# Kernel tuning notes

Measured on AMD Instinct MI355X. Metric: run time of the kernel, lower is better.

Reference implementation:

```python
import jax, jax.numpy as jnp
import numpy as np

N = 50000
E = 600000
IN_C = 128
HID = 128
OUT_C = 2


def setup_inputs() -> dict:
    key = jax.random.key(0)
    ks = jax.random.split(key, 16)
    x = jax.random.normal(ks[0], (N, IN_C), dtype=jnp.float32)
    edge_index = jax.random.randint(ks[1], (2, E), 0, N, dtype=jnp.int64)
    s = 0.05
    # policy_net: Linear(2*in, 64) -> ReLU -> Linear(64, 1) -> Sigmoid
    W_p1 = jax.random.normal(ks[2], (64, 2 * IN_C), dtype=jnp.float32) * s
    b_p1 = jnp.zeros((64,), dtype=jnp.float32)
    W_p2 = jax.random.normal(ks[3], (1, 64), dtype=jnp.float32) * s
    b_p2 = jnp.zeros((1,), dtype=jnp.float32)
    # GCNConv weights (lin without bias + separate bias, PyG convention)
    W1 = jax.random.normal(ks[4], (HID, IN_C), dtype=jnp.float32) * s
    b1 = jnp.zeros((HID,), dtype=jnp.float32)
    W2 = jax.random.normal(ks[5], (HID, HID), dtype=jnp.float32) * s
    b2 = jnp.zeros((HID,), dtype=jnp.float32)
    W_lin = jax.random.normal(ks[6], (OUT_C, HID), dtype=jnp.float32) * s
    b_lin = jnp.zeros((OUT_C,), dtype=jnp.float32)
    return {"x": x, "edge_index": edge_index, "W_p1": W_p1, "b_p1": b_p1,
            "W_p2": W_p2, "b_p2": b_p2, "W1": W1, "b1": b1, "W2": W2,
            "b2": b2, "W_lin": W_lin, "b_lin": b_lin}


def gcn_conv(x, src, dst, edge_weight, W, b, n_nodes):
    # PyG GCNConv with normalize=True, add_self_loops=True, given edge_weight.
    loop = jnp.arange(n_nodes, dtype=src.dtype)
    s = jnp.concatenate([src, loop])
    d = jnp.concatenate([dst, loop])
    w = jnp.concatenate([edge_weight, jnp.ones((n_nodes,), x.dtype)])
    deg = jax.ops.segment_sum(w, d, num_segments=n_nodes)
    dinv = jnp.where(deg > 0, jax.lax.rsqrt(jnp.where(deg > 0, deg, 1.0)), 0.0)
    norm = dinv[s] * w * dinv[d]  # [E+N]
    xl = x @ W.T  # [N, out]
    msg = norm[:, None] * xl[s]  # gather + scale
    agg = jax.ops.segment_sum(msg, d, num_segments=n_nodes)
    return agg + b


def reference(x, edge_index, W_p1, b_p1, W_p2, b_p2, W1, b1, W2, b2, W_lin, b_lin):
    src, dst = edge_index[0], edge_index[1]
    # edge-weight policy MLP on gathered, concatenated endpoint features
    cat_feat = jnp.concatenate([x[src], x[dst]], axis=1)  # [E, 2*in]
    h = jax.nn.relu(cat_feat @ W_p1.T + b_p1)
    edge_weight = jax.nn.sigmoid(h @ W_p2.T + b_p2)[:, 0]  # [E]
    x1 = jax.nn.relu(gcn_conv(x, src, dst, edge_weight, W1, b1, N))
    x2 = jax.nn.relu(gcn_conv(x1, src, dst, edge_weight, W2, b2, N))
    out = x2 @ W_lin.T + b_lin
    return jax.nn.sigmoid(out)
```

## Files before the change

### kernel.cpp

```cpp
#include <hip/hip_runtime.h>
#include <hip/hip_bf16.h>

#define NN 50000
#define NE 600000
#define CPAD 16

typedef __attribute__((ext_vector_type(8))) short short8;
typedef __attribute__((ext_vector_type(8))) _Float16 half8;
typedef __attribute__((ext_vector_type(4))) float floatx4;

__device__ __forceinline__ short bf16_bits(float v) {
    __hip_bfloat16 h = __float2bfloat16(v);
    return *reinterpret_cast<short*>(&h);
}

__device__ __forceinline__ void stage_w(const short* __restrict__ src, short* lds) {
    int t = threadIdx.x;
#pragma unroll
    for (int i = 0; i < 8; ++i) {
        int gci = t + i * 256;
        int row = gci >> 4, ci = gci & 15;
        short8 v = *(const short8*)(src + gci * 8);
        *(short8*)(lds + row * 128 + ((ci ^ (row & 7)) << 3)) = v;
    }
}

__global__ void k_init_cvt(const int* __restrict__ raw, int* __restrict__ count,
                           int* __restrict__ flag, int* __restrict__ bsums,
                           const float* __restrict__ wp1,
                           const float* __restrict__ w1, const float* __restrict__ w2,
                           __hip_bfloat16* __restrict__ wcatb, __hip_bfloat16* __restrict__ w1b,
                           __hip_bfloat16* __restrict__ w2b) {
    int i = blockIdx.x * blockDim.x + threadIdx.x;
    if (i < NN) {
        count[(size_t)i * CPAD] = 0;
    }
    if (i < 128) bsums[i] = 0;
    if (i < 16384) {
        int r = i >> 7, c = i & 127;
        float v = (r < 64) ? wp1[r * 256 + c] : wp1[(r - 64) * 256 + 128 + c];
        wcatb[i] = __float2bfloat16(v);
    } else if (i < 32768) {
        w1b[i - 16384] = __float2bfloat16(w1[i - 16384]);
    } else if (i < 49152) {
        w2b[i - 32768] = __float2bfloat16(w2[i - 32768]);
    }
    if (blockIdx.x == 0) {
        if (threadIdx.x == 0) *flag = 0;
        __syncthreads();
        int any = 0;
        for (int j = threadIdx.x; j < 1024; j += 256) any |= raw[2 * j + 1];
        if (any) atomicOr(flag, 1);
    }
}

#define GCNT 293
#define GG 782
__global__ __launch_bounds__(256) void k_uv_cnt(
    const float* __restrict__ x, const __hip_bfloat16* __restrict__ Wb,
    const float* __restrict__ bp1, _Float16* __restrict__ uvh,
    __hip_bfloat16* __restrict__ xb, const int* __restrict__ raw,
    const int* __restrict__ flag, int* __restrict__ count, int* __restrict__ rank) {
    if (blockIdx.x < GCNT) {
        const bool f32 = (*flag) != 0;
        const long long* r64 = (const long long*)raw;
        int gid = blockIdx.x * 256 + threadIdx.x;
        int e0 = gid * 8;
        if (e0 + 8 <= NE) {
            int dd[8];
            if (f32) {
#pragma unroll
                for (int k = 0; k < 8; ++k) dd[k] = raw[NE + e0 + k];
            } else {
#pragma unroll
                for (int k = 0; k < 8; ++k) dd[k] = (int)r64[NE + e0 + k];
            }
            int rk[8];
#pragma unroll
            for (int k = 0; k < 8; ++k) rk[k] = atomicAdd(&count[(size_t)dd[k] * CPAD], 1);
#pragma unroll
            for (int k = 0; k < 8; ++k) rank[e0 + k] = rk[k];
        } else {
            for (int e = e0; e < NE; ++e) {
                int d = f32 ? raw[NE + e] : (int)r64[NE + e];
                rank[e] = atomicAdd(&count[(size_t)d * CPAD], 1);
            }
        }
        return;
    }
    __shared__ short wlds[16384];
    stage_w((const short*)Wb, wlds);
    __syncthreads();

    const int lane = threadIdx.x & 63;
    const int wave = threadIdx.x >> 6;
    const int col = lane & 15;
    const int quad = lane >> 4;

    int tile = (blockIdx.x - GCNT) * 4 + wave;
    if (tile >= NN / 16) return;
    int base = tile * 16;

    short8 bfrag[4][8];
    const int rx = col & 7;
#pragma unroll
    for (int tt = 0; tt < 8; ++tt) {
        int row = tt * 16 + col;
#pragma unroll
        for (int kk = 0; kk < 4; ++kk)
            bfrag[kk][tt] = *(const short8*)(wlds + row * 128 + (((kk * 4 + quad) ^ rx) << 3));
    }

    floatx4 acc[8];
#pragma unroll
    for (int t = 0; t < 8; ++t) acc[t] = (floatx4){0.f, 0.f, 0.f, 0.f};
#pragma unroll
    for (int kk = 0; kk < 4; ++kk) {
        const float* xrow = x + (size_t)(base + col) * 128 + kk * 32 + quad * 8;
        float4 f0 = ((const float4*)xrow)[0];
        float4 f1 = ((const float4*)xrow)[1];
        short8 afrag;
        afrag[0] = bf16_bits(f0.x); afrag[1] = bf16_bits(f0.y);
        afrag[2] = bf16_bits(f0.z); afrag[3] = bf16_bits(f0.w);
        afrag[4] = bf16_bits(f1.x); afrag[5] = bf16_bits(f1.y);
        afrag[6] = bf16_bits(f1.z); afrag[7] = bf16_bits(f1.w);
        *(short8*)((short*)xb + (size_t)(base + col) * 128 + kk * 32 + quad * 8) = afrag;
#pragma unroll
        for (int tt = 0; tt < 8; ++tt)
            acc[tt] = __builtin_amdgcn_mfma_f32_16x16x32_bf16(afrag, bfrag[kk][tt], acc[tt], 0, 0, 0);
    }
#pragma unroll
    for (int tt = 0; tt < 8; ++tt) {
        int n = tt * 16 + col;
        float badd = (tt >= 4) ? bp1[n - 64] : 0.f;
#pragma unroll
        for (int r = 0; r < 4; ++r) {
            int row = base + quad * 4 + r;
            uvh[(size_t)row * 128 + n] = (_Float16)(acc[tt][r] + badd);
        }
    }
}

__global__ __launch_bounds__(512) void k_scan_rowptr(
    const int* __restrict__ count, int* __restrict__ bsums, int* __restrict__ rowptr) {
    __shared__ int s[512];
    __shared__ int red[512];
    int tid = threadIdx.x, bid = blockIdx.x;
    int i = bid * 512 + tid;
    s[tid] = (i < NN) ? count[(size_t)i * CPAD] : 0;
    __syncthreads();
    for (int off = 1; off < 512; off <<= 1) {
        int t = (tid >= off) ? s[tid - off] : 0;
        __syncthreads();
        s[tid] += t;
        __syncthreads();
    }
    if (tid == 511) atomicExch(&bsums[bid], s[511] + 1);
    int part = 0;
    for (int j = tid; j < bid; j += 512) {
        int v;
        do { v = atomicAdd(&bsums[j], 0); } while (v == 0);
        part += v - 1;
    }
    red[tid] = part;
    __syncthreads();
    for (int off = 256; off > 0; off >>= 1) {
        if (tid < off) red[tid] += red[tid + off];
        __syncthreads();
    }
    int prefix = red[0];
    if (i < NN) rowptr[i + 1] = s[tid] + prefix;
    if (bid == 0 && tid == 0) rowptr[0] = 0;
}

#define GPOL 9375
__global__ __launch_bounds__(256) void k_pol_fill(
    const int* __restrict__ raw, const int* __restrict__ flag,
    const int* __restrict__ rank, const int* __restrict__ rowptr,
    const _Float16* __restrict__ uvh, const float* __restrict__ wp2,
    const float* __restrict__ bp2, int2* __restrict__ meta) {
    const bool f32 = (*flag) != 0;
    const long long* r64 = (const long long*)raw;
    int pb = blockIdx.x;
    int wave = threadIdx.x >> 6, lane = threadIdx.x & 63;
    int g = lane >> 3, c = lane & 7;
    int e1 = pb * 64 + wave * 16 + g;
    int e2 = e1 + 8;
    int s1, d1, s2, d2;
    if (f32) {
        s1 = raw[e1]; d1 = raw[NE + e1];
        s2 = raw[e2]; d2 = raw[NE + e2];
    } else {
        s1 = (int)r64[e1]; d1 = (int)r64[NE + e1];
        s2 = (int)r64[e2]; d2 = (int)r64[NE + e2];
    }
    half8 u1 = *(const half8*)(uvh + (size_t)s1 * 128 + c * 8);
    half8 v1 = *(const half8*)(uvh + (size_t)d1 * 128 + 64 + c * 8);
    half8 u2 = *(const half8*)(uvh + (size_t)s2 * 128 + c * 8);
    half8 v2 = *(const half8*)(uvh + (size_t)d2 * 128 + 64 + c * 8);
    float w2v[8];
    const float4* w2p = (const float4*)(wp2 + c * 8);
    float4 wa = w2p[0], wb = w2p[1];
    w2v[0] = wa.x; w2v[1] = wa.y; w2v[2] = wa.z; w2v[3] = wa.w;
    w2v[4] = wb.x; w2v[5] = wb.y; w2v[6] = wb.z; w2v[7] = wb.w;
    float b2 = bp2[0];
    float p1 = 0.f, p2 = 0.f;
#pragma unroll
    for (int j = 0; j < 8; ++j) {
        float h1 = (float)u1[j] + (float)v1[j];
        float h2 = (float)u2[j] + (float)v2[j];
        h1 = h1 > 0.f ? h1 : 0.f;
        h2 = h2 > 0.f ? h2 : 0.f;
        p1 += h1 * w2v[j];
        p2 += h2 * w2v[j];
    }
    p1 += __shfl_xor(p1, 1, 64); p2 += __shfl_xor(p2, 1, 64);
    p1 += __shfl_xor(p1, 2, 64); p2 += __shfl_xor(p2, 2, 64);
    p1 += __shfl_xor(p1, 4, 64); p2 += __shfl_xor(p2, 4, 64);
    if (c == 0) {
        float ew1 = 1.f / (1.f + __expf(-(p1 + b2)));
        float ew2 = 1.f / (1.f + __expf(-(p2 + b2)));
        int rk1 = rank[e1], rk2 = rank[e2];
        int rb1 = rowptr[d1], rb2 = rowptr[d2];
        meta[rb1 + rk1] = make_int2(s1, __float_as_int(ew1));
        meta[rb2 + rk2] = make_int2(s2, __float_as_int(ew2));
    }
}

template <bool CDEG>
__global__ __launch_bounds__(256) void k_gemm(
    const __hip_bfloat16* __restrict__ A, const __hip_bfloat16* __restrict__ Wb,
    const int* __restrict__ rowptr, const int2* __restrict__ meta,
    float* __restrict__ deg, _Float16* __restrict__ xlh) {
    __shared__ short wlds[16384];
    stage_w((const short*)Wb, wlds);
    __syncthreads();

    const int lane = threadIdx.x & 63;
    const int wave = threadIdx.x >> 6;
    const int col = lane & 15;
    const int quad = lane >> 4;

    int tile = blockIdx.x * 4 + wave;
    if (tile >= NN / 16) return;
    int base = tile * 16;

    short8 bfrag[4][8];
    const int rx = col & 7;
#pragma unroll
    for (int tt = 0; tt < 8; ++tt) {
        int row = tt * 16 + col;
#pragma unroll
        for (int kk = 0; kk < 4; ++kk)
            bfrag[kk][tt] = *(const short8*)(wlds + row * 128 + (((kk * 4 + quad) ^ rx) << 3));
    }
    const short* xs = (const short*)A;

    floatx4 acc[8];
#pragma unroll
    for (int t = 0; t < 8; ++t) acc[t] = (floatx4){0.f, 0.f, 0.f, 0.f};
#pragma unroll
    for (int kk = 0; kk < 4; ++kk) {
        short8 afrag = *(const short8*)(xs + (size_t)(base + col) * 128 + kk * 32 + quad * 8);
#pragma unroll
        for (int tt = 0; tt < 8; ++tt)
            acc[tt] = __builtin_amdgcn_mfma_f32_16x16x32_bf16(afrag, bfrag[kk][tt], acc[tt], 0, 0, 0);
    }
    float di[4];
    if (CDEG) {
        int rn = base + col;
        int beg = rowptr[rn], end = rowptr[rn + 1];
        float sdeg = 0.f;
        for (int p = beg + quad; p < end; p += 4) sdeg += __int_as_float(meta[p].y);
        sdeg += __shfl_xor(sdeg, 16, 64);
        sdeg += __shfl_xor(sdeg, 32, 64);
        float dv = 1.f + sdeg;
        if (quad == 0) deg[rn] = dv;
#pragma unroll
        for (int r = 0; r < 4; ++r) di[r] = rsqrtf(__shfl(dv, quad * 4 + r, 64));
    } else {
#pragma unroll
        for (int r = 0; r < 4; ++r) di[r] = rsqrtf(deg[base + quad * 4 + r]);
    }
#pragma unroll
    for (int tt = 0; tt < 8; ++tt) {
        int n = tt * 16 + col;
#pragma unroll
        for (int r = 0; r < 4; ++r) {
            int row = base + quad * 4 + r;
            xlh[(size_t)row * 128 + n] = (_Float16)(di[r] * acc[tt][r]);
        }
    }
}

__device__ __forceinline__ void scatter_core(
    const int* __restrict__ rowptr, const int2* __restrict__ meta,
    const _Float16* __restrict__ xlh, int wid, int g, int c, float acc[8]) {
    int beg = rowptr[wid], end = rowptr[wid + 1];
    for (int p = beg + g; p < end; p += 16) {
        int2 m1 = meta[p];
        int2 m2 = (p + 4  < end) ? meta[p + 4]  : make_int2(m1.x, 0);
        int2 m3 = (p + 8  < end) ? meta[p + 8]  : make_int2(m1.x, 0);
        int2 m4 = (p + 12 < end) ? meta[p + 12] : make_int2(m1.x, 0);
        half8 r1 = *(const half8*)(xlh + (size_t)m1.x * 128 + c * 8);
        half8 r2 = *(const half8*)(xlh + (size_t)m2.x * 128 + c * 8);
        half8 r3 = *(const half8*)(xlh + (size_t)m3.x * 128 + c * 8);
        half8 r4 = *(const half8*)(xlh + (size_t)m4.x * 128 + c * 8);
        float c1 = __int_as_float(m1.y), c2 = __int_as_float(m2.y);
        float c3 = __int_as_float(m3.y), c4 = __int_as_float(m4.y);
#pragma unroll
        for (int j = 0; j < 8; ++j)
            acc[j] += c1 * (float)r1[j] + c2 * (float)r2[j] + c3 * (float)r3[j] + c4 * (float)r4[j];
    }
#pragma unroll
    for (int j = 0; j < 8; ++j) {
        acc[j] += __shfl_xor(acc[j], 16, 64);
        acc[j] += __shfl_xor(acc[j], 32, 64);
    }
}

__global__ __launch_bounds__(256) void k_scatter_mid(
    const int* __restrict__ rowptr, const int2* __restrict__ meta,
    const float* __restrict__ deg, const _Float16* __restrict__ xlh,
    const float* __restrict__ bias, __hip_bfloat16* __restrict__ xb2) {
    int wid = (blockIdx.x * blockDim.x + threadIdx.x) >> 6;
    int lane = threadIdx.x & 63;
    if (wid >= NN) return;
    int g = lane >> 4, c = lane & 15;
    float acc[8] = {0.f, 0.f, 0.f, 0.f, 0.f, 0.f, 0.f, 0.f};
    scatter_core(rowptr, meta, xlh, wid, g, c, acc);
    if (g == 0) {
        float dn = rsqrtf(deg[wid]);
        half8 sv = *(const half8*)(xlh + (size_t)wid * 128 + c * 8);
        const float4* bp = (const float4*)(bias + c * 8);
        float4 ba = bp[0], bb = bp[1];
        float bv[8] = {ba.x, ba.y, ba.z, ba.w, bb.x, bb.y, bb.z, bb.w};
        short8 o;
#pragma unroll
        for (int j = 0; j < 8; ++j) {
            float t = bv[j] + dn * ((float)sv[j] + acc[j]);
            t = t > 0.f ? t : 0.f;
            o[j] = bf16_bits(t);
        }
        *(short8*)((short*)xb2 + (size_t)wid * 128 + c * 8) = o;
    }
}

__global__ __launch_bounds__(256) void k_scatter_out(
    const int* __restrict__ rowptr, const int2* __restrict__ meta,
    const float* __restrict__ deg, const _Float16* __restrict__ xlh,
    const float* __restrict__ bias, const float* __restrict__ wlin,
    const float* __restrict__ blin, float* __restrict__ out) {
    int wid = (blockIdx.x * blockDim.x + threadIdx.x) >> 6;
    int lane = threadIdx.x & 63;
    if (wid >= NN) return;
    int g = lane >> 4, c = lane & 15;
    float acc[8] = {0.f, 0.f, 0.f, 0.f, 0.f, 0.f, 0.f, 0.f};
    scatter_core(rowptr, meta, xlh, wid, g, c, acc);
    if (g == 0) {
        float dn = rsqrtf(deg[wid]);
        half8 sv = *(const half8*)(xlh + (size_t)wid * 128 + c * 8);
        const float4* bp = (const float4*)(bias + c * 8);
        float4 ba = bp[0], bb = bp[1];
        float bv[8] = {ba.x, ba.y, ba.z, ba.w, bb.x, bb.y, bb.z, bb.w};
        float p0 = 0.f, p1 = 0.f;
#pragma unroll
        for (int j = 0; j < 8; ++j) {
            float t = bv[j] + dn * ((float)sv[j] + acc[j]);
            t = t > 0.f ? t : 0.f;
            p0 += t * wlin[c * 8 + j];
            p1 += t * wlin[128 + c * 8 + j];
        }
#pragma unroll
        for (int off = 1; off < 16; off <<= 1) {
            p0 += __shfl_xor(p0, off, 64);
            p1 += __shfl_xor(p1, off, 64);
        }
        if (c == 0) {
            out[wid * 2 + 0] = 1.f / (1.f + __expf(-(p0 + blin[0])));
            out[wid * 2 + 1] = 1.f / (1.f + __expf(-(p1 + blin[1])));
        }
    }
}


extern "C" void kernel_launch(void* const* d_in, const int* in_sizes, int n_in,
                              void* d_out, int out_size, void* d_ws, size_t ws_size,
                              hipStream_t stream) {
    const float* x = (const float*)d_in[0];
    const int* eidx_raw = (const int*)d_in[1];
    const float* W_p1 = (const float*)d_in[2];
    const float* b_p1 = (const float*)d_in[3];
    const float* W_p2 = (const float*)d_in[4];
    const float* b_p2 = (const float*)d_in[5];
    const float* W1 = (const float*)d_in[6];
    const float* b1 = (const float*)d_in[7];
    const float* W2 = (const float*)d_in[8];
    const float* b2 = (const float*)d_in[9];
    const float* W_lin = (const float*)d_in[10];
    const float* b_lin = (const float*)d_in[11];
    float* out = (float*)d_out;

    char* ws = (char*)d_ws;
    size_t off = 0;
    auto alloc = [&](size_t bytes) -> void* {
        off = (off + 255) & ~(size_t)255;
        void* p = ws + off;
        off += bytes;
        return p;
    };
    float* deg = (float*)alloc(NN * 4);
    int* rowptr = (int*)alloc((NN + 1) * 4);
    int* count = (int*)alloc((size_t)NN * CPAD * 4);
    int* flag = (int*)alloc(4);
    int* bsums = (int*)alloc(128 * 4);
    int* rank = (int*)alloc((size_t)NE * 4);
    int2* meta = (int2*)alloc((size_t)NE * 8);
    __hip_bfloat16* xb = (__hip_bfloat16*)alloc((size_t)NN * 128 * 2);
    _Float16* xlh = (_Float16*)alloc((size_t)NN * 128 * 2);
    _Float16* uvh = (_Float16*)alloc((size_t)NN * 128 * 2);
    __hip_bfloat16* wcatb = (__hip_bfloat16*)alloc(128 * 128 * 2);
    __hip_bfloat16* w1b = (__hip_bfloat16*)alloc(128 * 128 * 2);
    __hip_bfloat16* w2b = (__hip_bfloat16*)alloc(128 * 128 * 2);

    const int TB = 256;
    int gN = (NN + TB - 1) / TB;
    int gS = (NN + 3) / 4;

    k_init_cvt<<<gN, TB, 0, stream>>>(eidx_raw, count, flag, bsums, W_p1, W1, W2, wcatb, w1b, w2b);
    k_uv_cnt<<<GCNT + GG, TB, 0, stream>>>(x, wcatb, b_p1, uvh, xb, eidx_raw, flag, count, rank);
    k_scan_rowptr<<<98, 512, 0, stream>>>(count, bsums, rowptr);
    k_pol_fill<<<GPOL, TB, 0, stream>>>(eidx_raw, flag, rank, rowptr, uvh, W_p2, b_p2, meta);
    k_gemm<true><<<GG, TB, 0, stream>>>(xb, w1b, rowptr, meta, deg, xlh);
    k_scatter_mid<<<gS, TB, 0, stream>>>(rowptr, meta, deg, xlh, b1, xb);
    k_gemm<false><<<GG, TB, 0, stream>>>(xb, w2b, rowptr, meta, deg, xlh);
    k_scatter_out<<<gS, TB, 0, stream>>>(rowptr, meta, deg, xlh, b2, W_lin, b_lin, out);
}
```

Before: 235.5 us.

## Fuse first GCN GEMM into policy GEMM kernel and compute degrees via atomics

```diff
diff --git a/kernel.cpp b/kernel.cpp
--- a/kernel.cpp
+++ b/kernel.cpp
@@ -26,14 +26,15 @@
 }
 
 __global__ void k_init_cvt(const int* __restrict__ raw, int* __restrict__ count,
-                           int* __restrict__ flag, int* __restrict__ bsums,
-                           const float* __restrict__ wp1,
+                           float* __restrict__ degp, int* __restrict__ flag,
+                           int* __restrict__ bsums, const float* __restrict__ wp1,
                            const float* __restrict__ w1, const float* __restrict__ w2,
                            __hip_bfloat16* __restrict__ wcatb, __hip_bfloat16* __restrict__ w1b,
                            __hip_bfloat16* __restrict__ w2b) {
     int i = blockIdx.x * blockDim.x + threadIdx.x;
     if (i < NN) {
         count[(size_t)i * CPAD] = 0;
+        degp[(size_t)i * CPAD] = 1.0f;
     }
     if (i < 128) bsums[i] = 0;
     if (i < 16384) {
@@ -54,32 +55,33 @@
     }
 }
 
-#define GCNT 293
+#define GCNT 147
 #define GG 782
 __global__ __launch_bounds__(256) void k_uv_cnt(
-    const float* __restrict__ x, const __hip_bfloat16* __restrict__ Wb,
-    const float* __restrict__ bp1, _Float16* __restrict__ uvh,
-    __hip_bfloat16* __restrict__ xb, const int* __restrict__ raw,
-    const int* __restrict__ flag, int* __restrict__ count, int* __restrict__ rank) {
+    const float* __restrict__ x, const __hip_bfloat16* __restrict__ Wcat,
+    const __hip_bfloat16* __restrict__ W1b, const float* __restrict__ bp1,
+    _Float16* __restrict__ uvh, _Float16* __restrict__ xlh,
+    const int* __restrict__ raw, const int* __restrict__ flag,
+    int* __restrict__ count, int* __restrict__ rank) {
     if (blockIdx.x < GCNT) {
         const bool f32 = (*flag) != 0;
         const long long* r64 = (const long long*)raw;
         int gid = blockIdx.x * 256 + threadIdx.x;
-        int e0 = gid * 8;
-        if (e0 + 8 <= NE) {
-            int dd[8];
+        int e0 = gid * 16;
+        if (e0 + 16 <= NE) {
+            int dd[16];
             if (f32) {
 #pragma unroll
-                for (int k = 0; k < 8; ++k) dd[k] = raw[NE + e0 + k];
+                for (int k = 0; k < 16; ++k) dd[k] = raw[NE + e0 + k];
             } else {
 #pragma unroll
-                for (int k = 0; k < 8; ++k) dd[k] = (int)r64[NE + e0 + k];
-            }
-            int rk[8];
-#pragma unroll
-            for (int k = 0; k < 8; ++k) rk[k] = atomicAdd(&count[(size_t)dd[k] * CPAD], 1);
-#pragma unroll
-            for (int k = 0; k < 8; ++k) rank[e0 + k] = rk[k];
+                for (int k = 0; k < 16; ++k) dd[k] = (int)r64[NE + e0 + k];
+            }
+            int rk[16];
+#pragma unroll
+            for (int k = 0; k < 16; ++k) rk[k] = atomicAdd(&count[(size_t)dd[k] * CPAD], 1);
+#pragma unroll
+            for (int k = 0; k < 16; ++k) rank[e0 + k] = rk[k];
         } else {
             for (int e = e0; e < NE; ++e) {
                 int d = f32 ? raw[NE + e] : (int)r64[NE + e];
@@ -89,54 +91,79 @@
         return;
     }
     __shared__ short wlds[16384];
-    stage_w((const short*)Wb, wlds);
+    stage_w((const short*)Wcat, wlds);
     __syncthreads();
 
     const int lane = threadIdx.x & 63;
     const int wave = threadIdx.x >> 6;
     const int col = lane & 15;
     const int quad = lane >> 4;
+    const int rx = col & 7;
 
     int tile = (blockIdx.x - GCNT) * 4 + wave;
-    if (tile >= NN / 16) return;
+    if (tile >= NN / 16) tile = NN / 16 - 1;
     int base = tile * 16;
 
-    short8 bfrag[4][8];
-    const int rx = col & 7;
-#pragma unroll
-    for (int tt = 0; tt < 8; ++tt) {
-        int row = tt * 16 + col;
-#pragma unroll
-        for (int kk = 0; kk < 4; ++kk)
-            bfrag[kk][tt] = *(const short8*)(wlds + row * 128 + (((kk * 4 + quad) ^ rx) << 3));
-    }
-
-    floatx4 acc[8];
-#pragma unroll
-    for (int t = 0; t < 8; ++t) acc[t] = (floatx4){0.f, 0.f, 0.f, 0.f};
+    short8 af[4];
 #pragma unroll
     for (int kk = 0; kk < 4; ++kk) {
         const float* xrow = x + (size_t)(base + col) * 128 + kk * 32 + quad * 8;
         float4 f0 = ((const float4*)xrow)[0];
         float4 f1 = ((const float4*)xrow)[1];
-        short8 afrag;
-        afrag[0] = bf16_bits(f0.x); afrag[1] = bf16_bits(f0.y);
-        afrag[2] = bf16_bits(f0.z); afrag[3] = bf16_bits(f0.w);
-        afrag[4] = bf16_bits(f1.x); afrag[5] = bf16_bits(f1.y);
-        afrag[6] = bf16_bits(f1.z); afrag[7] = bf16_bits(f1.w);
-        *(short8*)((short*)xb + (size_t)(base + col) * 128 + kk * 32 + quad * 8) = afrag;
-#pragma unroll
-        for (int tt = 0; tt < 8; ++tt)
-            acc[tt] = __builtin_amdgcn_mfma_f32_16x16x32_bf16(afrag, bfrag[kk][tt], acc[tt], 0, 0, 0);
-    }
-#pragma unroll
-    for (int tt = 0; tt < 8; ++tt) {
-        int n = tt * 16 + col;
-        float badd = (tt >= 4) ? bp1[n - 64] : 0.f;
-#pragma unroll
-        for (int r = 0; r < 4; ++r) {
-            int row = base + quad * 4 + r;
-            uvh[(size_t)row * 128 + n] = (_Float16)(acc[tt][r] + badd);
+        short8 a;
+        a[0] = bf16_bits(f0.x); a[1] = bf16_bits(f0.y);
+        a[2] = bf16_bits(f0.z); a[3] = bf16_bits(f0.w);
+        a[4] = bf16_bits(f1.x); a[5] = bf16_bits(f1.y);
+        a[6] = bf16_bits(f1.z); a[7] = bf16_bits(f1.w);
+        af[kk] = a;
+    }
+
+    {
+        floatx4 acc[8];
+#pragma unroll
+        for (int t = 0; t < 8; ++t) acc[t] = (floatx4){0.f, 0.f, 0.f, 0.f};
+#pragma unroll
+        for (int kk = 0; kk < 4; ++kk) {
+#pragma unroll
+            for (int tt = 0; tt < 8; ++tt) {
+                short8 b = *(const short8*)(wlds + (tt * 16 + col) * 128 + (((kk * 4 + quad) ^ rx) << 3));
+                acc[tt] = __builtin_amdgcn_mfma_f32_16x16x32_bf16(af[kk], b, acc[tt], 0, 0, 0);
+            }
+        }
+#pragma unroll
+        for (int tt = 0; tt < 8; ++tt) {
+            int n = tt * 16 + col;
+            float badd = (tt >= 4) ? bp1[n - 64] : 0.f;
+#pragma unroll
+            for (int r = 0; r < 4; ++r) {
+                int row = base + quad * 4 + r;
+                uvh[(size_t)row * 128 + n] = (_Float16)(acc[tt][r] + badd);
+            }
+        }
+    }
+    __syncthreads();
+    stage_w((const short*)W1b, wlds);
+    __syncthreads();
+    {
+        floatx4 acc[8];
+#pragma unroll
+        for (int t = 0; t < 8; ++t) acc[t] = (floatx4){0.f, 0.f, 0.f, 0.f};
+#pragma unroll
+        for (int kk = 0; kk < 4; ++kk) {
+#pragma unroll
+            for (int tt = 0; tt < 8; ++tt) {
+                short8 b = *(const short8*)(wlds + (tt * 16 + col) * 128 + (((kk * 4 + quad) ^ rx) << 3));
+                acc[tt] = __builtin_amdgcn_mfma_f32_16x16x32_bf16(af[kk], b, acc[tt], 0, 0, 0);
+            }
+        }
+#pragma unroll
+        for (int tt = 0; tt < 8; ++tt) {
+            int n = tt * 16 + col;
+#pragma unroll
+            for (int r = 0; r < 4; ++r) {
+                int row = base + quad * 4 + r;
+                xlh[(size_t)row * 128 + n] = (_Float16)(acc[tt][r]);
+            }
         }
     }
 }
@@ -178,7 +205,7 @@
     const int* __restrict__ raw, const int* __restrict__ flag,
     const int* __restrict__ rank, const int* __restrict__ rowptr,
     const _Float16* __restrict__ uvh, const float* __restrict__ wp2,
-    const float* __restrict__ bp2, int2* __restrict__ meta) {
+    const float* __restrict__ bp2, int2* __restrict__ meta, float* __restrict__ degp) {
     const bool f32 = (*flag) != 0;
     const long long* r64 = (const long long*)raw;
     int pb = blockIdx.x;
@@ -224,14 +251,14 @@
         int rb1 = rowptr[d1], rb2 = rowptr[d2];
         meta[rb1 + rk1] = make_int2(s1, __float_as_int(ew1));
         meta[rb2 + rk2] = make_int2(s2, __float_as_int(ew2));
-    }
-}
-
-template <bool CDEG>
-__global__ __launch_bounds__(256) void k_gemm(
+        atomicAdd(&degp[(size_t)d1 * CPAD], ew1);
+        atomicAdd(&degp[(size_t)d2 * CPAD], ew2);
+    }
+}
+
+__global__ __launch_bounds__(256) void k_gemm2(
     const __hip_bfloat16* __restrict__ A, const __hip_bfloat16* __restrict__ Wb,
-    const int* __restrict__ rowptr, const int2* __restrict__ meta,
-    float* __restrict__ deg, _Float16* __restrict__ xlh) {
+    const float* __restrict__ degp, _Float16* __restrict__ xlh) {
     __shared__ short wlds[16384];
     stage_w((const short*)Wb, wlds);
     __syncthreads();
@@ -267,21 +294,8 @@
             acc[tt] = __builtin_amdgcn_mfma_f32_16x16x32_bf16(afrag, bfrag[kk][tt], acc[tt], 0, 0, 0);
     }
     float di[4];
-    if (CDEG) {
-        int rn = base + col;
-        int beg = rowptr[rn], end = rowptr[rn + 1];
-        float sdeg = 0.f;
-        for (int p = beg + quad; p < end; p += 4) sdeg += __int_as_float(meta[p].y);
-        sdeg += __shfl_xor(sdeg, 16, 64);
-        sdeg += __shfl_xor(sdeg, 32, 64);
-        float dv = 1.f + sdeg;
-        if (quad == 0) deg[rn] = dv;
-#pragma unroll
-        for (int r = 0; r < 4; ++r) di[r] = rsqrtf(__shfl(dv, quad * 4 + r, 64));
-    } else {
-#pragma unroll
-        for (int r = 0; r < 4; ++r) di[r] = rsqrtf(deg[base + quad * 4 + r]);
-    }
+#pragma unroll
+    for (int r = 0; r < 4; ++r) di[r] = rsqrtf(degp[(size_t)(base + quad * 4 + r) * CPAD]);
 #pragma unroll
     for (int tt = 0; tt < 8; ++tt) {
         int n = tt * 16 + col;
@@ -290,6 +304,37 @@
             int row = base + quad * 4 + r;
             xlh[(size_t)row * 128 + n] = (_Float16)(di[r] * acc[tt][r]);
         }
+    }
+}
+
+__device__ __forceinline__ void scatter_core_u(
+    const int* __restrict__ rowptr, const int2* __restrict__ meta,
+    const float* __restrict__ degp, const _Float16* __restrict__ xlh,
+    int wid, int g, int c, float acc[8]) {
+    int beg = rowptr[wid], end = rowptr[wid + 1];
+    for (int p = beg + g; p < end; p += 16) {
+        int2 m1 = meta[p];
+        int2 m2 = (p + 4  < end) ? meta[p + 4]  : make_int2(m1.x, 0);
+        int2 m3 = (p + 8  < end) ? meta[p + 8]  : make_int2(m1.x, 0);
+        int2 m4 = (p + 12 < end) ? meta[p + 12] : make_int2(m1.x, 0);
+        half8 r1 = *(const half8*)(xlh + (size_t)m1.x * 128 + c * 8);
+        half8 r2 = *(const half8*)(xlh + (size_t)m2.x * 128 + c * 8);
+        half8 r3 = *(const half8*)(xlh + (size_t)m3.x * 128 + c * 8);
+        half8 r4 = *(const half8*)(xlh + (size_t)m4.x * 128 + c * 8);
+        float dv1 = degp[(size_t)m1.x * CPAD], dv2 = degp[(size_t)m2.x * CPAD];
+        float dv3 = degp[(size_t)m3.x * CPAD], dv4 = degp[(size_t)m4.x * CPAD];
+        float c1 = __int_as_float(m1.y) * rsqrtf(dv1);
+        float c2 = __int_as_float(m2.y) * rsqrtf(dv2);
+        float c3 = __int_as_float(m3.y) * rsqrtf(dv3);
+        float c4 = __int_as_float(m4.y) * rsqrtf(dv4);
+#pragma unroll
+        for (int j = 0; j < 8; ++j)
+            acc[j] += c1 * (float)r1[j] + c2 * (float)r2[j] + c3 * (float)r3[j] + c4 * (float)r4[j];
+    }
+#pragma unroll
+    for (int j = 0; j < 8; ++j) {
+        acc[j] += __shfl_xor(acc[j], 16, 64);
+        acc[j] += __shfl_xor(acc[j], 32, 64);
     }
 }
 
@@ -321,16 +366,16 @@
 
 __global__ __launch_bounds__(256) void k_scatter_mid(
     const int* __restrict__ rowptr, const int2* __restrict__ meta,
-    const float* __restrict__ deg, const _Float16* __restrict__ xlh,
+    const float* __restrict__ degp, const _Float16* __restrict__ xlh,
     const float* __restrict__ bias, __hip_bfloat16* __restrict__ xb2) {
     int wid = (blockIdx.x * blockDim.x + threadIdx.x) >> 6;
     int lane = threadIdx.x & 63;
     if (wid >= NN) return;
     int g = lane >> 4, c = lane & 15;
     float acc[8] = {0.f, 0.f, 0.f, 0.f, 0.f, 0.f, 0.f, 0.f};
-    scatter_core(rowptr, meta, xlh, wid, g, c, acc);
+    scatter_core_u(rowptr, meta, degp, xlh, wid, g, c, acc);
     if (g == 0) {
-        float dn = rsqrtf(deg[wid]);
+        float dn = rsqrtf(degp[(size_t)wid * CPAD]);
         half8 sv = *(const half8*)(xlh + (size_t)wid * 128 + c * 8);
         const float4* bp = (const float4*)(bias + c * 8);
         float4 ba = bp[0], bb = bp[1];
@@ -338,7 +383,7 @@
         short8 o;
 #pragma unroll
         for (int j = 0; j < 8; ++j) {
-            float t = bv[j] + dn * ((float)sv[j] + acc[j]);
+            float t = bv[j] + dn * (dn * (float)sv[j] + acc[j]);
             t = t > 0.f ? t : 0.f;
             o[j] = bf16_bits(t);
         }
@@ -348,7 +393,7 @@
 
 __global__ __launch_bounds__(256) void k_scatter_out(
     const int* __restrict__ rowptr, const int2* __restrict__ meta,
-    const float* __restrict__ deg, const _Float16* __restrict__ xlh,
+    const float* __restrict__ degp, const _Float16* __restrict__ xlh,
     const float* __restrict__ bias, const float* __restrict__ wlin,
     const float* __restrict__ blin, float* __restrict__ out) {
     int wid = (blockIdx.x * blockDim.x + threadIdx.x) >> 6;
@@ -358,7 +403,7 @@
     float acc[8] = {0.f, 0.f, 0.f, 0.f, 0.f, 0.f, 0.f, 0.f};
     scatter_core(rowptr, meta, xlh, wid, g, c, acc);
     if (g == 0) {
-        float dn = rsqrtf(deg[wid]);
+        float dn = rsqrtf(degp[(size_t)wid * CPAD]);
         half8 sv = *(const half8*)(xlh + (size_t)wid * 128 + c * 8);
         const float4* bp = (const float4*)(bias + c * 8);
         float4 ba = bp[0], bb = bp[1];
@@ -409,14 +454,14 @@
         off += bytes;
         return p;
     };
-    float* deg = (float*)alloc(NN * 4);
+    float* degp = (float*)alloc((size_t)NN * CPAD * 4);
     int* rowptr = (int*)alloc((NN + 1) * 4);
     int* count = (int*)alloc((size_t)NN * CPAD * 4);
     int* flag = (int*)alloc(4);
     int* bsums = (int*)alloc(128 * 4);
     int* rank = (int*)alloc((size_t)NE * 4);
     int2* meta = (int2*)alloc((size_t)NE * 8);
-    __hip_bfloat16* xb = (__hip_bfloat16*)alloc((size_t)NN * 128 * 2);
+    __hip_bfloat16* xb2 = (__hip_bfloat16*)alloc((size_t)NN * 128 * 2);
     _Float16* xlh = (_Float16*)alloc((size_t)NN * 128 * 2);
     _Float16* uvh = (_Float16*)alloc((size_t)NN * 128 * 2);
     __hip_bfloat16* wcatb = (__hip_bfloat16*)alloc(128 * 128 * 2);
@@ -427,12 +472,14 @@
     int gN = (NN + TB - 1) / TB;
     int gS = (NN + 3) / 4;
 
-    k_init_cvt<<<gN, TB, 0, stream>>>(eidx_raw, count, flag, bsums, W_p1, W1, W2, wcatb, w1b, w2b);
-    k_uv_cnt<<<GCNT + GG, TB, 0, stream>>>(x, wcatb, b_p1, uvh, xb, eidx_raw, flag, count, rank);
+    k_init_cvt<<<gN, TB, 0, stream>>>(eidx_raw, count, degp, flag, bsums, W_p1, W1, W2,
+                                      wcatb, w1b, w2b);
+    k_uv_cnt<<<GCNT + GG, TB, 0, stream>>>(x, wcatb, w1b, b_p1, uvh, xlh, eidx_raw, flag,
+                                           count, rank);
     k_scan_rowptr<<<98, 512, 0, stream>>>(count, bsums, rowptr);
-    k_pol_fill<<<GPOL, TB, 0, stream>>>(eidx_raw, flag, rank, rowptr, uvh, W_p2, b_p2, meta);
-    k_gemm<true><<<GG, TB, 0, stream>>>(xb, w1b, rowptr, meta, deg, xlh);
-    k_scatter_mid<<<gS, TB, 0, stream>>>(rowptr, meta, deg, xlh, b1, xb);
-    k_gemm<false><<<GG, TB, 0, stream>>>(xb, w2b, rowptr, meta, deg, xlh);
-    k_scatter_out<<<gS, TB, 0, stream>>>(rowptr, meta, deg, xlh, b2, W_lin, b_lin, out);
-}
+    k_pol_fill<<<GPOL, TB, 0, stream>>>(eidx_raw, flag, rank, rowptr, uvh, W_p2, b_p2,
+                                        meta, degp);
+    k_scatter_mid<<<gS, TB, 0, stream>>>(rowptr, meta, degp, xlh, b1, xb2);
+    k_gemm2<<<GG, TB, 0, stream>>>(xb2, w2b, degp, xlh);
+    k_scatter_out<<<gS, TB, 0, stream>>>(rowptr, meta, degp, xlh, b2, W_lin, b_lin, out);
+}
```

Result: slower. 243.1 us (+3.2%).
